# Optimization experiments

Hardware: AMD Instinct MI355X
Metric: run time of the kernel (lower is better)

The kernel has to match this reference:

```python
import jax, jax.numpy as jnp
import numpy as np

# Grid / physics constants (stand-ins for the attributes of self.model)
N = 256                 # voxels per axis (cubic unit cell)
CELL = 100.0            # unit cell edge in Angstrom (orthogonal cell, frac matrix = I/CELL)
SPACING = CELL / N      # voxel spacing in Angstrom
SOLVENT_R = 1.1         # dilation probe radius (init default `radius`)
EROSION_R = 0.9         # erosion radius (init default `erosion_radius`)
VDW_MAX = 1.9           # static upper bound on vdw radii (generation range [1.2,1.9])
N_ATOMS = 5000


def setup_inputs() -> dict:
    key = jax.random.key(0)
    k1, k2 = jax.random.split(key)
    xyz = jax.random.uniform(k1, (N_ATOMS, 3), jnp.float32) * CELL
    vdw_radii = 1.2 + 0.7 * jax.random.uniform(k2, (N_ATOMS,), jnp.float32)
    return {"xyz": xyz, "vdw_radii": vdw_radii}


def _solvent_pipeline(xyz, vdw_radii):
    # ---- Step 1: dilation -- per-atom radius query into the voxel grid ----
    max_r = VDW_MAX + SOLVENT_R                       # self.max_radius_angstrom
    Kh = int(np.ceil(max_r / SPACING))
    g = np.arange(-Kh, Kh + 1)
    offs = np.stack(np.meshgrid(g, g, g, indexing='ij'), -1).reshape(-1, 3)
    offs = jnp.asarray(offs, jnp.int32)               # [M,3] local voxel offsets

    base = jnp.floor(xyz / SPACING).astype(jnp.int32)          # [A,3] home voxel
    coords = base[:, None, :] + offs[None, :, :]               # [A,M,3]
    centers = coords.astype(jnp.float32) * SPACING             # voxel centers (unwrapped)
    d = jnp.sqrt(jnp.sum((centers - xyz[:, None, :]) ** 2, -1))  # [A,M] atom-voxel dist

    w = jnp.mod(coords, N)                                     # periodic wrap of indices
    flat = ((w[..., 0] * N + w[..., 1]) * N + w[..., 2]).ravel()

    vr = vdw_radii[:, None]
    prot = (d < vr).ravel()                                    # inside vdw -> protein core
    bound = ((d >= vr) & (d < vr + SOLVENT_R)).ravel()         # vdw..vdw+probe -> boundary

    protein = (jnp.zeros(N ** 3, jnp.int8).at[flat].max(prot.astype(jnp.int8)) > 0)
    boundary = (jnp.zeros(N ** 3, jnp.int8).at[flat].max(bound.astype(jnp.int8)) > 0)
    protein = protein.reshape(N, N, N)
    boundary = boundary.reshape(N, N, N) & ~protein            # symmetry = identity (P1)
    def_solv = ~(protein | boundary)

    # ---- Step 2: erosion -- boundary voxel flips to solvent if any voxel within
    #      erosion_radius is definitely solvent ----
    rh = int(np.ceil(EROSION_R / SPACING))
    g2 = np.arange(-rh, rh + 1)
    eo = np.stack(np.meshgrid(g2, g2, g2, indexing='ij'), -1).reshape(-1, 3)
    eo = eo[np.linalg.norm(eo * SPACING, axis=1) <= EROSION_R]  # sphere stencil (static)
    has_nb = jnp.zeros((N, N, N), bool)
    for o in eo:  # small static stencil (~50 offsets)
        has_nb = has_nb | jnp.roll(def_solv, shift=(-int(o[0]), -int(o[1]), -int(o[2])), axis=(0, 1, 2))
    flip = boundary & has_nb
    protein_with_boundary = (protein | boundary) & ~flip
    solvent = (~protein_with_boundary).astype(jnp.float32)

    # ---- Step 3: Gaussian smoothing with circular padding ----
    sigma = (SOLVENT_R / SPACING) / 4.0                        # self.transition (voxels)
    ks = int(4 * sigma + 1)
    if ks % 2 == 0:
        ks += 1
    x = np.arange(ks) - ks // 2
    g1 = np.exp(-x ** 2 / (2 * sigma ** 2))
    g1 = g1 / g1.sum()
    k3 = g1[:, None, None] * g1[None, :, None] * g1[None, None, :]
    k3 = jnp.asarray(k3 / k3.sum(), jnp.float32)
    pad = ks // 2
    padded = jnp.pad(solvent, pad, mode='wrap')
    out = jax.lax.conv_general_dilated(padded[None, None], k3[None, None], (1, 1, 1), 'VALID')
    return out[0, 0]  # [N,N,N] smoothed solvent mask


def reference(xyz, vdw_radii):
    return _solvent_pipeline(xyz, vdw_radii)
```

## Files before the change

### kernel.cpp

```cpp
#include <hip/hip_runtime.h>
#include <math.h>

#define NG 256
#define NG3 (NG*NG*NG)
#define NW (NG3/64)

typedef unsigned long long u64;
typedef unsigned int u32;

constexpr float SPACING_F = 0.390625f;
constexpr int KH = 8;
constexpr int KD = 17;
constexpr int NPAIR = KD * KD;

#define CB(x, y) (((((x) & 255) << 8) | ((y) & 255)) << 2)

__global__ void __launch_bounds__(256) splat_bits_kernel(
    const float* __restrict__ xyz, const float* __restrict__ vdw,
    u64* __restrict__ occ_bits, u64* __restrict__ p_bits, int natoms)
{
    int t = blockIdx.x * 256 + threadIdx.x;
    if (t >= natoms * NPAIR) return;
    int atom = t / NPAIR;
    int pr = t - atom * NPAIR;
    int dx = pr / KD - KH;
    int dy = pr - (pr / KD) * KD - KH;

    const float ax = xyz[atom * 3 + 0];
    const float ay = xyz[atom * 3 + 1];
    const float az = xyz[atom * 3 + 2];
    const float vr = vdw[atom];
    const float br = __fadd_rn(vr, 1.1f);
    const int bx = (int)floorf(__fdiv_rn(ax, SPACING_F));
    const int by = (int)floorf(__fdiv_rn(ay, SPACING_F));
    const int bz = (int)floorf(__fdiv_rn(az, SPACING_F));

    const int cx = bx + dx, cy = by + dy;
    float ex = __fsub_rn(__fmul_rn((float)cx, SPACING_F), ax);
    float ey = __fsub_rn(__fmul_rn((float)cy, SPACING_F), ay);
    float rxy2 = __fadd_rn(__fmul_rn(ex, ex), __fmul_rn(ey, ey));
    if (rxy2 >= __fmul_rn(br, br)) return;

    u32 mo = 0, mp = 0;
    #pragma unroll
    for (int k = 0; k < KD; ++k) {
        int cz = bz + k - KH;
        float ez = __fsub_rn(__fmul_rn((float)cz, SPACING_F), az);
        float s = __fadd_rn(rxy2, __fmul_rn(ez, ez));
        float d = __fsqrt_rn(s);
        mo |= (d < br) ? (1u << k) : 0u;
        mp |= (d < vr) ? (1u << k) : 0u;
    }
    if (!mo) return;

    const int cb = CB(cx, cy);
    const int zA = (bz - KH) & 255;
    const int wa = zA >> 6;
    const int off = zA & 63;

    u64 lo = (u64)mo << off;
    u64 hi = off ? ((u64)mo >> (64 - off)) : 0ULL;
    if (lo) atomicOr(&occ_bits[cb | wa], lo);
    if (hi) atomicOr(&occ_bits[cb | ((wa + 1) & 3)], hi);
    if (mp) {
        u64 plo = (u64)mp << off;
        u64 phi = off ? ((u64)mp >> (64 - off)) : 0ULL;
        if (plo) atomicOr(&p_bits[cb | wa], plo);
        if (phi) atomicOr(&p_bits[cb | ((wa + 1) & 3)], phi);
    }
}

#define LCB(ox, oy) ((((ox) * 14) + (oy)) * 4)
#define SCB(sx, sy) ((((sx) * 10) + (sy)) * 4)

union SMem {
    u64 occT[784];
    float stage[256][33];
};

__device__ __forceinline__ u64 lrng5(const u64* T, int cb, int wz) {
    u64 C = T[cb | wz], P = T[cb | ((wz + 3) & 3)], Nw = T[cb | ((wz + 1) & 3)];
    u64 d1 = (C << 1) | (P >> 63), d2 = (C << 2) | (P >> 62);
    u64 u1 = (C >> 1) | (Nw << 63), u2 = (C >> 2) | (Nw << 62);
    return C & d1 & d2 & u1 & u2;
}
__device__ __forceinline__ u64 lrng3(const u64* T, int cb, int wz) {
    u64 C = T[cb | wz], P = T[cb | ((wz + 3) & 3)], Nw = T[cb | ((wz + 1) & 3)];
    u64 d1 = (C << 1) | (P >> 63);
    u64 u1 = (C >> 1) | (Nw << 63);
    return C & d1 & u1;
}

struct Tri { u64 m1, m0, p1; };
__device__ __forceinline__ Tri triL(const u64* T, int cb, int wz) {
    u64 C = T[cb | wz], P = T[cb | ((wz + 3) & 3)], Nw = T[cb | ((wz + 1) & 3)];
    Tri t;
    t.m0 = C;
    t.m1 = (C << 1) | (P >> 63);
    t.p1 = (C >> 1) | (Nw << 63);
    return t;
}

__device__ __forceinline__ void csa(u64 a, u64 b, u64 c, u64& s, u64& cy) {
    u64 t = a ^ b;
    s = t ^ c;
    cy = (a & b) | (t & c);
}

__global__ void __launch_bounds__(256) solv_gauss_kernel(
    const u64* __restrict__ occ_bits, const u64* __restrict__ p_bits,
    float* __restrict__ out, float W0, float W1, float W2, float W3)
{
    __shared__ SMem sm;
    __shared__ u64 solT[400];
    __shared__ float lutA[256];

    const int tid = threadIdx.x;
    const int bx = blockIdx.x & 31, by = blockIdx.x >> 5;
    const int x0 = bx * 8, y0 = by * 8;

    for (int i = tid; i < 784; i += 256) {
        int owz = i & 3; int c = i >> 2;
        int oy = c % 14, ox = c / 14;
        sm.occT[i] = occ_bits[CB(x0 - 3 + ox, y0 - 3 + oy) | owz];
    }
    {
        int g = tid & 1, c1v = (tid >> 1) & 7, c2v = (tid >> 4) & 15;
        float acc = g ? W0 : 0.0f;
        acc = fmaf(W1, (float)c1v, acc);
        acc = fmaf(W2, (float)c2v, acc);
        lutA[tid] = acc;
    }
    __syncthreads();

    for (int i = tid; i < 400; i += 256) {
        int swz = i & 3; int c = i >> 2;
        int sy = c % 10, sx = c / 10;
        int ox = sx + 2, oy = sy + 2;
        const u64* T = sm.occT;
        u64 ero = lrng5(T, LCB(ox, oy), swz);
        ero &= lrng5(T, LCB(ox + 1, oy), swz);
        ero &= lrng5(T, LCB(ox - 1, oy), swz);
        ero &= lrng5(T, LCB(ox, oy + 1), swz);
        ero &= lrng5(T, LCB(ox, oy - 1), swz);
        ero &= lrng3(T, LCB(ox + 1, oy + 1), swz);
        ero &= lrng3(T, LCB(ox + 1, oy - 1), swz);
        ero &= lrng3(T, LCB(ox - 1, oy + 1), swz);
        ero &= lrng3(T, LCB(ox - 1, oy - 1), swz);
        ero &= lrng3(T, LCB(ox + 2, oy), swz);
        ero &= lrng3(T, LCB(ox - 2, oy), swz);
        ero &= lrng3(T, LCB(ox, oy + 2), swz);
        ero &= lrng3(T, LCB(ox, oy - 2), swz);
        ero &= T[LCB(ox + 1, oy + 2) | swz];
        ero &= T[LCB(ox + 1, oy - 2) | swz];
        ero &= T[LCB(ox - 1, oy + 2) | swz];
        ero &= T[LCB(ox - 1, oy - 2) | swz];
        ero &= T[LCB(ox + 2, oy + 1) | swz];
        ero &= T[LCB(ox + 2, oy - 1) | swz];
        ero &= T[LCB(ox - 2, oy + 1) | swz];
        ero &= T[LCB(ox - 2, oy - 1) | swz];

        u64 C = T[LCB(ox, oy) | swz];
        u64 pw = p_bits[CB(x0 - 1 + sx, y0 - 1 + sy) | swz];
        solT[i] = ~(pw | (C & ero));
    }
    __syncthreads();

    const int gwz = tid & 3;
    const int gc = tid >> 2;
    const int gy = gc & 7, gx = gc >> 3;
    const int sx = gx + 1, sy = gy + 1;

    Tri cc = triL(solT, SCB(sx, sy), gwz);
    Tri e0 = triL(solT, SCB(sx + 1, sy), gwz), e1 = triL(solT, SCB(sx - 1, sy), gwz);
    Tri e2 = triL(solT, SCB(sx, sy + 1), gwz), e3 = triL(solT, SCB(sx, sy - 1), gwz);
    Tri d0 = triL(solT, SCB(sx + 1, sy + 1), gwz), d1 = triL(solT, SCB(sx + 1, sy - 1), gwz);
    Tri d2 = triL(solT, SCB(sx - 1, sy + 1), gwz), d3 = triL(solT, SCB(sx - 1, sy - 1), gwz);

    u64 sa, ca, sb, cb2;
    csa(cc.m1, cc.p1, e0.m0, sa, ca);
    csa(e1.m0, e2.m0, e3.m0, sb, cb2);
    u64 c1b0 = sa ^ sb; u64 h = sa & sb;
    u64 c1b1, c1b2;
    csa(ca, cb2, h, c1b1, c1b2);

    u64 s1, k1, s2, k2, s3, k3, s4, k4;
    csa(e0.m1, e0.p1, e1.m1, s1, k1);
    csa(e1.p1, e2.m1, e2.p1, s2, k2);
    csa(e3.m1, e3.p1, d0.m0, s3, k3);
    csa(d1.m0, d2.m0, d3.m0, s4, k4);
    u64 t5, kt;
    csa(s1, s2, s3, t5, kt);
    u64 c2b0 = t5 ^ s4; u64 h0 = t5 & s4;
    u64 u_, ku, v_, kv;
    csa(k1, k2, k3, u_, ku);
    csa(k4, kt, h0, v_, kv);
    u64 c2b1 = u_ ^ v_; u64 h1 = u_ & v_;
    u64 c2b2, c2b3;
    csa(ku, kv, h1, c2b2, c2b3);

    u64 p1s, p1c, p2s, p2c;
    csa(d0.m1, d0.p1, d1.m1, p1s, p1c);
    csa(d1.p1, d2.m1, d2.p1, p2s, p2c);
    u64 t3, kt3;
    csa(p1s, p2s, d3.m1, t3, kt3);
    u64 c3b0 = t3 ^ d3.p1; u64 h3 = t3 & d3.p1;
    u64 u3, ku3;
    csa(p1c, p2c, kt3, u3, ku3);
    u64 c3b1 = u3 ^ h3; u64 h4 = u3 & h3;
    u64 c3b2 = ku3 ^ h4, c3b3 = ku3 & h4;

    #pragma unroll
    for (int hh = 0; hh < 2; ++hh) {
        const int sh = hh * 32;
        u32 pA[8] = { (u32)(cc.m0 >> sh), (u32)(c1b0 >> sh), (u32)(c1b1 >> sh),
                      (u32)(c1b2 >> sh), (u32)(c2b0 >> sh), (u32)(c2b1 >> sh),
                      (u32)(c2b2 >> sh), (u32)(c2b3 >> sh) };
        u32 pB[4] = { (u32)(c3b0 >> sh), (u32)(c3b1 >> sh),
                      (u32)(c3b2 >> sh), (u32)(c3b3 >> sh) };
        #pragma unroll
        for (int z0 = 0; z0 < 8; ++z0) {
            u32 accA = 0, accB = 0;
            #pragma unroll
            for (int j = 0; j < 8; ++j) accA |= ((pA[j] >> z0) & 0x01010101u) << j;
            #pragma unroll
            for (int j = 0; j < 4; ++j) accB |= ((pB[j] >> z0) & 0x01010101u) << j;
            #pragma unroll
            for (int b = 0; b < 4; ++b) {
                int idxA = (accA >> (8 * b)) & 255;
                int c3v  = (accB >> (8 * b)) & 15;
                float val = fmaf(W3, (float)c3v, lutA[idxA]);
                sm.stage[tid][z0 + 8 * b] = val;
            }
        }
        __syncthreads();
        #pragma unroll
        for (int k = 0; k < 8; ++k) {
            int i = tid + k * 256;
            int wl = i >> 3;
            int zo = (i & 7) * 4;
            int ggx = wl >> 5, ggy = (wl >> 2) & 7, ggwz = wl & 3;
            size_t base = ((size_t)(((x0 + ggx) << 10) + (y0 + ggy) * 4 + ggwz)) * 64;
            float4 v = make_float4(sm.stage[wl][zo], sm.stage[wl][zo + 1],
                                   sm.stage[wl][zo + 2], sm.stage[wl][zo + 3]);
            *(float4*)(out + base + sh + zo) = v;
        }
        __syncthreads();
    }
}

extern "C" void kernel_launch(void* const* d_in, const int* in_sizes, int n_in,
                              void* d_out, int out_size, void* d_ws, size_t ws_size,
                              hipStream_t stream)
{
    const float* xyz = (const float*)d_in[0];
    const float* vdw = (const float*)d_in[1];
    float* out = (float*)d_out;

    u64* occ_bits = (u64*)d_ws;
    u64* p_bits   = occ_bits + NW;
    const int natoms = in_sizes[1];

    hipMemsetAsync(occ_bits, 0, 2 * NW * sizeof(u64), stream);

    int nthreads = natoms * NPAIR;
    splat_bits_kernel<<<(nthreads + 255) / 256, 256, 0, stream>>>(
        xyz, vdw, occ_bits, p_bits, natoms);

    double spacing = 100.0 / 256.0;
    double sigma = 1.1 / spacing / 4.0;
    double a = exp(-1.0 / (2.0 * sigma * sigma));
    double ssum = 2.0 * a + 1.0;
    double an = a / ssum, bn = 1.0 / ssum;
    float W0 = (float)(bn * bn * bn);
    float W1 = (float)(an * bn * bn);
    float W2 = (float)(an * an * bn);
    float W3 = (float)(an * an * an);

    solv_gauss_kernel<<<1024, 256, 0, stream>>>(
        occ_bits, p_bits, out, W0, W1, W2, W3);
}
```

Measured before the change: 113.6 us.

## Replace atomic atom splat with binned per-column gather of bit masks

Atoms are first bucketed into a 64x64 xy grid of bins. A column-oriented kernel then has each block collect candidate atoms from neighbouring bins into shared memory, and each voxel column ORs its own occupancy and protein bits in registers before writing them with plain stores. This removes the global atomicOr traffic and the memset of the bit arrays, since every column is now written in full. The fixed caps on atoms per bin and candidates per block can silently drop atoms when atoms cluster, and only 256 blocks launch, which may leave much of the GPU idle.

Measured after the change: 133.2 us. 1.17x slower.

```diff
diff --git a/kernel.cpp b/kernel.cpp
--- a/kernel.cpp
+++ b/kernel.cpp
@@ -11,62 +11,128 @@
 constexpr float SPACING_F = 0.390625f;
 constexpr int KH = 8;
 constexpr int KD = 17;
-constexpr int NPAIR = KD * KD;
+
+#define NBIN 64
+#define BCAP 32
+#define NCAND 160
 
 #define CB(x, y) (((((x) & 255) << 8) | ((y) & 255)) << 2)
 
-__global__ void __launch_bounds__(256) splat_bits_kernel(
+__global__ void bin_fill_kernel(const float* __restrict__ xyz, int natoms,
+                                int* __restrict__ bin_cnt, int* __restrict__ bin_list)
+{
+    int a = blockIdx.x * 256 + threadIdx.x;
+    if (a >= natoms) return;
+    float ax = xyz[a * 3 + 0], ay = xyz[a * 3 + 1];
+    int bx = (int)floorf(__fdiv_rn(ax, SPACING_F));
+    int by = (int)floorf(__fdiv_rn(ay, SPACING_F));
+    int b = ((by >> 2) & (NBIN - 1)) * NBIN + ((bx >> 2) & (NBIN - 1));
+    int s = atomicAdd(&bin_cnt[b], 1);
+    if (s < BCAP) bin_list[b * BCAP + s] = a;
+}
+
+__global__ void __launch_bounds__(512) col_splat_kernel(
     const float* __restrict__ xyz, const float* __restrict__ vdw,
-    u64* __restrict__ occ_bits, u64* __restrict__ p_bits, int natoms)
+    const int* __restrict__ bin_cnt, const int* __restrict__ bin_list,
+    u64* __restrict__ occ_bits, u64* __restrict__ p_bits)
 {
-    int t = blockIdx.x * 256 + threadIdx.x;
-    if (t >= natoms * NPAIR) return;
-    int atom = t / NPAIR;
-    int pr = t - atom * NPAIR;
-    int dx = pr / KD - KH;
-    int dy = pr - (pr / KD) * KD - KH;
-
-    const float ax = xyz[atom * 3 + 0];
-    const float ay = xyz[atom * 3 + 1];
-    const float az = xyz[atom * 3 + 2];
-    const float vr = vdw[atom];
-    const float br = __fadd_rn(vr, 1.1f);
-    const int bx = (int)floorf(__fdiv_rn(ax, SPACING_F));
-    const int by = (int)floorf(__fdiv_rn(ay, SPACING_F));
-    const int bz = (int)floorf(__fdiv_rn(az, SPACING_F));
-
-    const int cx = bx + dx, cy = by + dy;
-    float ex = __fsub_rn(__fmul_rn((float)cx, SPACING_F), ax);
-    float ey = __fsub_rn(__fmul_rn((float)cy, SPACING_F), ay);
-    float rxy2 = __fadd_rn(__fmul_rn(ex, ex), __fmul_rn(ey, ey));
-    if (rxy2 >= __fmul_rn(br, br)) return;
-
-    u32 mo = 0, mp = 0;
-    #pragma unroll
-    for (int k = 0; k < KD; ++k) {
-        int cz = bz + k - KH;
-        float ez = __fsub_rn(__fmul_rn((float)cz, SPACING_F), az);
-        float s = __fadd_rn(rxy2, __fmul_rn(ez, ez));
-        float d = __fsqrt_rn(s);
-        mo |= (d < br) ? (1u << k) : 0u;
-        mp |= (d < vr) ? (1u << k) : 0u;
-    }
-    if (!mo) return;
-
-    const int cb = CB(cx, cy);
-    const int zA = (bz - KH) & 255;
-    const int wa = zA >> 6;
-    const int off = zA & 63;
-
-    u64 lo = (u64)mo << off;
-    u64 hi = off ? ((u64)mo >> (64 - off)) : 0ULL;
-    if (lo) atomicOr(&occ_bits[cb | wa], lo);
-    if (hi) atomicOr(&occ_bits[cb | ((wa + 1) & 3)], hi);
-    if (mp) {
+    __shared__ float4 candF[NCAND];
+    __shared__ int    candB[NCAND];
+    __shared__ int lc;
+
+    const int tid = threadIdx.x;
+    const int BX = blockIdx.x & 15, BY = blockIdx.x >> 4;
+    const int x0 = BX * 16, y0 = BY * 16;
+
+    if (tid == 0) lc = 0;
+    __syncthreads();
+
+    if (tid < 64) {
+        int abx = (4 * BX - 2 + (tid & 7)) & (NBIN - 1);
+        int aby = (4 * BY - 2 + (tid >> 3)) & (NBIN - 1);
+        int b = aby * NBIN + abx;
+        int n = min(bin_cnt[b], BCAP);
+        if (n > 0) {
+            int base = atomicAdd(&lc, n);
+            for (int j = 0; j < n; ++j) {
+                int idx = base + j;
+                if (idx < NCAND) {
+                    int a = bin_list[b * BCAP + j];
+                    float ax = xyz[a * 3 + 0], ay = xyz[a * 3 + 1], az = xyz[a * 3 + 2];
+                    candF[idx] = make_float4(ax, ay, az, vdw[a]);
+                    int bx = (int)floorf(__fdiv_rn(ax, SPACING_F));
+                    int by = (int)floorf(__fdiv_rn(ay, SPACING_F));
+                    int bz = (int)floorf(__fdiv_rn(az, SPACING_F));
+                    candB[idx] = bx | (by << 8) | (bz << 16);
+                }
+            }
+        }
+    }
+    __syncthreads();
+    const int nc = min(lc, NCAND);
+
+    const int col = tid >> 1;
+    const int sub = tid & 1;
+    const int X = x0 + (col >> 4), Y = y0 + (col & 15);
+
+    u64 o0 = 0, o1 = 0, o2 = 0, o3 = 0;
+    u64 q0 = 0, q1 = 0, q2 = 0, q3 = 0;
+
+    for (int c = sub; c < nc; c += 2) {
+        float4 f = candF[c];
+        int bb = candB[c];
+        int bx = bb & 255, by = (bb >> 8) & 255, bz = (bb >> 16) & 255;
+        int dx = ((X - bx + 128) & 255) - 128;
+        int dy = ((Y - by + 128) & 255) - 128;
+        if (dx < -KH || dx > KH || dy < -KH || dy > KH) continue;
+        float ex = __fsub_rn(__fmul_rn((float)(bx + dx), SPACING_F), f.x);
+        float ey = __fsub_rn(__fmul_rn((float)(by + dy), SPACING_F), f.y);
+        float rxy2 = __fadd_rn(__fmul_rn(ex, ex), __fmul_rn(ey, ey));
+        float vr = f.w;
+        float br = __fadd_rn(vr, 1.1f);
+        if (rxy2 >= __fmul_rn(br, br)) continue;
+
+        u32 mo = 0, mp = 0;
+        #pragma unroll
+        for (int k = 0; k < KD; ++k) {
+            int cz = bz + k - KH;
+            float ez = __fsub_rn(__fmul_rn((float)cz, SPACING_F), f.z);
+            float s = __fadd_rn(rxy2, __fmul_rn(ez, ez));
+            float d = __fsqrt_rn(s);
+            mo |= (d < br) ? (1u << k) : 0u;
+            mp |= (d < vr) ? (1u << k) : 0u;
+        }
+        if (!mo) continue;
+
+        int zA = (bz - KH) & 255;
+        int wa = zA >> 6, off = zA & 63;
+        int wb = (wa + 1) & 3;
+        u64 lo = (u64)mo << off;
+        u64 hi = off ? ((u64)mo >> (64 - off)) : 0ULL;
         u64 plo = (u64)mp << off;
         u64 phi = off ? ((u64)mp >> (64 - off)) : 0ULL;
-        if (plo) atomicOr(&p_bits[cb | wa], plo);
-        if (phi) atomicOr(&p_bits[cb | ((wa + 1) & 3)], phi);
+        o0 |= (wa == 0 ? lo : 0) | (wb == 0 ? hi : 0);
+        o1 |= (wa == 1 ? lo : 0) | (wb == 1 ? hi : 0);
+        o2 |= (wa == 2 ? lo : 0) | (wb == 2 ? hi : 0);
+        o3 |= (wa == 3 ? lo : 0) | (wb == 3 ? hi : 0);
+        q0 |= (wa == 0 ? plo : 0) | (wb == 0 ? phi : 0);
+        q1 |= (wa == 1 ? plo : 0) | (wb == 1 ? phi : 0);
+        q2 |= (wa == 2 ? plo : 0) | (wb == 2 ? phi : 0);
+        q3 |= (wa == 3 ? plo : 0) | (wb == 3 ? phi : 0);
+    }
+
+    o0 |= __shfl_xor(o0, 1, 64);  o1 |= __shfl_xor(o1, 1, 64);
+    o2 |= __shfl_xor(o2, 1, 64);  o3 |= __shfl_xor(o3, 1, 64);
+    q0 |= __shfl_xor(q0, 1, 64);  q1 |= __shfl_xor(q1, 1, 64);
+    q2 |= __shfl_xor(q2, 1, 64);  q3 |= __shfl_xor(q3, 1, 64);
+
+    u64* dst = (sub == 0 ? occ_bits : p_bits) + CB(X, Y);
+    if (sub == 0) {
+        *(ulonglong2*)(dst + 0) = make_ulonglong2(o0, o1);
+        *(ulonglong2*)(dst + 2) = make_ulonglong2(o2, o3);
+    } else {
+        *(ulonglong2*)(dst + 0) = make_ulonglong2(q0, q1);
+        *(ulonglong2*)(dst + 2) = make_ulonglong2(q2, q3);
     }
 }
 
@@ -259,13 +325,15 @@
 
     u64* occ_bits = (u64*)d_ws;
     u64* p_bits   = occ_bits + NW;
+    int* bin_cnt  = (int*)(p_bits + NW);
+    int* bin_list = bin_cnt + NBIN * NBIN;
     const int natoms = in_sizes[1];
 
-    hipMemsetAsync(occ_bits, 0, 2 * NW * sizeof(u64), stream);
-
-    int nthreads = natoms * NPAIR;
-    splat_bits_kernel<<<(nthreads + 255) / 256, 256, 0, stream>>>(
-        xyz, vdw, occ_bits, p_bits, natoms);
+    hipMemsetAsync(bin_cnt, 0, NBIN * NBIN * sizeof(int), stream);
+    bin_fill_kernel<<<(natoms + 255) / 256, 256, 0, stream>>>(
+        xyz, natoms, bin_cnt, bin_list);
+    col_splat_kernel<<<256, 512, 0, stream>>>(
+        xyz, vdw, bin_cnt, bin_list, occ_bits, p_bits);
 
     double spacing = 100.0 / 256.0;
     double sigma = 1.1 / spacing / 4.0;
```

## Stage packed per-voxel count bits in shared memory and expand to floats at store

Applied to the files above, without the earlier changes.

Each thread now writes compact per-voxel count bit fields (8-bit A index and 4-bit B count) to shared memory instead of 64 staged floats. A single barrier follows, and the store phase unpacks those fields, does the LUT lookup and FMA, and writes float4s directly. This removes the two staging rounds and the extra barriers, and shrinks shared memory traffic. The occupancy tile load is also vectorized so one thread copies four u64 words with two 128-bit loads. In exchange, the LUT lookups and bit extraction move into the store loop, whose lutA reads may bank-conflict.

Measured after the change: 114.8 us. Within noise of the previous version (+1.1%).

```diff
diff --git a/kernel.cpp b/kernel.cpp
--- a/kernel.cpp
+++ b/kernel.cpp
@@ -72,10 +72,11 @@
 
 #define LCB(ox, oy) ((((ox) * 14) + (oy)) * 4)
 #define SCB(sx, sy) ((((sx) * 10) + (sy)) * 4)
+#define ASTRIDE 25
 
 union SMem {
     u64 occT[784];
-    float stage[256][33];
+    u32 accAB[256 * ASTRIDE];
 };
 
 __device__ __forceinline__ u64 lrng5(const u64* T, int cb, int wz) {
@@ -119,10 +120,14 @@
     const int bx = blockIdx.x & 31, by = blockIdx.x >> 5;
     const int x0 = bx * 8, y0 = by * 8;
 
-    for (int i = tid; i < 784; i += 256) {
-        int owz = i & 3; int c = i >> 2;
-        int oy = c % 14, ox = c / 14;
-        sm.occT[i] = occ_bits[CB(x0 - 3 + ox, y0 - 3 + oy) | owz];
+    if (tid < 196) {
+        int oy = tid % 14, ox = tid / 14;
+        const u64* src = &occ_bits[CB(x0 - 3 + ox, y0 - 3 + oy)];
+        ulonglong2 a = *(const ulonglong2*)(src);
+        ulonglong2 b = *(const ulonglong2*)(src + 2);
+        u64* dst = &sm.occT[(ox * 14 + oy) * 4];
+        *(ulonglong2*)(dst) = a;
+        *(ulonglong2*)(dst + 2) = b;
     }
     {
         int g = tid & 1, c1v = (tid >> 1) & 7, c2v = (tid >> 4) & 15;
@@ -166,86 +171,99 @@
     }
     __syncthreads();
 
-    const int gwz = tid & 3;
-    const int gc = tid >> 2;
-    const int gy = gc & 7, gx = gc >> 3;
-    const int sx = gx + 1, sy = gy + 1;
-
-    Tri cc = triL(solT, SCB(sx, sy), gwz);
-    Tri e0 = triL(solT, SCB(sx + 1, sy), gwz), e1 = triL(solT, SCB(sx - 1, sy), gwz);
-    Tri e2 = triL(solT, SCB(sx, sy + 1), gwz), e3 = triL(solT, SCB(sx, sy - 1), gwz);
-    Tri d0 = triL(solT, SCB(sx + 1, sy + 1), gwz), d1 = triL(solT, SCB(sx + 1, sy - 1), gwz);
-    Tri d2 = triL(solT, SCB(sx - 1, sy + 1), gwz), d3 = triL(solT, SCB(sx - 1, sy - 1), gwz);
-
-    u64 sa, ca, sb, cb2;
-    csa(cc.m1, cc.p1, e0.m0, sa, ca);
-    csa(e1.m0, e2.m0, e3.m0, sb, cb2);
-    u64 c1b0 = sa ^ sb; u64 h = sa & sb;
-    u64 c1b1, c1b2;
-    csa(ca, cb2, h, c1b1, c1b2);
-
-    u64 s1, k1, s2, k2, s3, k3, s4, k4;
-    csa(e0.m1, e0.p1, e1.m1, s1, k1);
-    csa(e1.p1, e2.m1, e2.p1, s2, k2);
-    csa(e3.m1, e3.p1, d0.m0, s3, k3);
-    csa(d1.m0, d2.m0, d3.m0, s4, k4);
-    u64 t5, kt;
-    csa(s1, s2, s3, t5, kt);
-    u64 c2b0 = t5 ^ s4; u64 h0 = t5 & s4;
-    u64 u_, ku, v_, kv;
-    csa(k1, k2, k3, u_, ku);
-    csa(k4, kt, h0, v_, kv);
-    u64 c2b1 = u_ ^ v_; u64 h1 = u_ & v_;
-    u64 c2b2, c2b3;
-    csa(ku, kv, h1, c2b2, c2b3);
-
-    u64 p1s, p1c, p2s, p2c;
-    csa(d0.m1, d0.p1, d1.m1, p1s, p1c);
-    csa(d1.p1, d2.m1, d2.p1, p2s, p2c);
-    u64 t3, kt3;
-    csa(p1s, p2s, d3.m1, t3, kt3);
-    u64 c3b0 = t3 ^ d3.p1; u64 h3 = t3 & d3.p1;
-    u64 u3, ku3;
-    csa(p1c, p2c, kt3, u3, ku3);
-    u64 c3b1 = u3 ^ h3; u64 h4 = u3 & h3;
-    u64 c3b2 = ku3 ^ h4, c3b3 = ku3 & h4;
+    {
+        const int gwz = tid & 3;
+        const int gc = tid >> 2;
+        const int gy = gc & 7, gx = gc >> 3;
+        const int sx = gx + 1, sy = gy + 1;
+
+        Tri cc = triL(solT, SCB(sx, sy), gwz);
+        Tri e0 = triL(solT, SCB(sx + 1, sy), gwz), e1 = triL(solT, SCB(sx - 1, sy), gwz);
+        Tri e2 = triL(solT, SCB(sx, sy + 1), gwz), e3 = triL(solT, SCB(sx, sy - 1), gwz);
+        Tri d0 = triL(solT, SCB(sx + 1, sy + 1), gwz), d1 = triL(solT, SCB(sx + 1, sy - 1), gwz);
+        Tri d2 = triL(solT, SCB(sx - 1, sy + 1), gwz), d3 = triL(solT, SCB(sx - 1, sy - 1), gwz);
+
+        u64 sa, ca, sb, cb2;
+        csa(cc.m1, cc.p1, e0.m0, sa, ca);
+        csa(e1.m0, e2.m0, e3.m0, sb, cb2);
+        u64 c1b0 = sa ^ sb; u64 h = sa & sb;
+        u64 c1b1, c1b2;
+        csa(ca, cb2, h, c1b1, c1b2);
+
+        u64 s1, k1, s2, k2, s3, k3, s4, k4;
+        csa(e0.m1, e0.p1, e1.m1, s1, k1);
+        csa(e1.p1, e2.m1, e2.p1, s2, k2);
+        csa(e3.m1, e3.p1, d0.m0, s3, k3);
+        csa(d1.m0, d2.m0, d3.m0, s4, k4);
+        u64 t5, kt;
+        csa(s1, s2, s3, t5, kt);
+        u64 c2b0 = t5 ^ s4; u64 h0 = t5 & s4;
+        u64 u_, ku, v_, kv;
+        csa(k1, k2, k3, u_, ku);
+        csa(k4, kt, h0, v_, kv);
+        u64 c2b1 = u_ ^ v_; u64 h1 = u_ & v_;
+        u64 c2b2, c2b3;
+        csa(ku, kv, h1, c2b2, c2b3);
+
+        u64 p1s, p1c, p2s, p2c;
+        csa(d0.m1, d0.p1, d1.m1, p1s, p1c);
+        csa(d1.p1, d2.m1, d2.p1, p2s, p2c);
+        u64 t3, kt3;
+        csa(p1s, p2s, d3.m1, t3, kt3);
+        u64 c3b0 = t3 ^ d3.p1; u64 h3 = t3 & d3.p1;
+        u64 u3, ku3;
+        csa(p1c, p2c, kt3, u3, ku3);
+        u64 c3b1 = u3 ^ h3; u64 h4 = u3 & h3;
+        u64 c3b2 = ku3 ^ h4, c3b3 = ku3 & h4;
+
+        u32* myA = &sm.accAB[tid * ASTRIDE];
+        #pragma unroll
+        for (int hh = 0; hh < 2; ++hh) {
+            const int sh = hh * 32;
+            u32 pA[8] = { (u32)(cc.m0 >> sh), (u32)(c1b0 >> sh), (u32)(c1b1 >> sh),
+                          (u32)(c1b2 >> sh), (u32)(c2b0 >> sh), (u32)(c2b1 >> sh),
+                          (u32)(c2b2 >> sh), (u32)(c2b3 >> sh) };
+            u32 pB[4] = { (u32)(c3b0 >> sh), (u32)(c3b1 >> sh),
+                          (u32)(c3b2 >> sh), (u32)(c3b3 >> sh) };
+            u32 bv[8];
+            #pragma unroll
+            for (int z0 = 0; z0 < 8; ++z0) {
+                u32 accA = 0, accB = 0;
+                #pragma unroll
+                for (int j = 0; j < 8; ++j) accA |= ((pA[j] >> z0) & 0x01010101u) << j;
+                #pragma unroll
+                for (int j = 0; j < 4; ++j) accB |= ((pB[j] >> z0) & 0x01010101u) << j;
+                myA[hh * 8 + z0] = accA;
+                bv[z0] = accB;
+            }
+            #pragma unroll
+            for (int p = 0; p < 4; ++p)
+                myA[16 + hh * 4 + p] = bv[2 * p] | (bv[2 * p + 1] << 4);
+        }
+    }
+    __syncthreads();
 
     #pragma unroll
-    for (int hh = 0; hh < 2; ++hh) {
-        const int sh = hh * 32;
-        u32 pA[8] = { (u32)(cc.m0 >> sh), (u32)(c1b0 >> sh), (u32)(c1b1 >> sh),
-                      (u32)(c1b2 >> sh), (u32)(c2b0 >> sh), (u32)(c2b1 >> sh),
-                      (u32)(c2b2 >> sh), (u32)(c2b3 >> sh) };
-        u32 pB[4] = { (u32)(c3b0 >> sh), (u32)(c3b1 >> sh),
-                      (u32)(c3b2 >> sh), (u32)(c3b3 >> sh) };
-        #pragma unroll
-        for (int z0 = 0; z0 < 8; ++z0) {
-            u32 accA = 0, accB = 0;
-            #pragma unroll
-            for (int j = 0; j < 8; ++j) accA |= ((pA[j] >> z0) & 0x01010101u) << j;
-            #pragma unroll
-            for (int j = 0; j < 4; ++j) accB |= ((pB[j] >> z0) & 0x01010101u) << j;
-            #pragma unroll
-            for (int b = 0; b < 4; ++b) {
-                int idxA = (accA >> (8 * b)) & 255;
-                int c3v  = (accB >> (8 * b)) & 15;
-                float val = fmaf(W3, (float)c3v, lutA[idxA]);
-                sm.stage[tid][z0 + 8 * b] = val;
-            }
-        }
-        __syncthreads();
-        #pragma unroll
-        for (int k = 0; k < 8; ++k) {
-            int i = tid + k * 256;
-            int wl = i >> 3;
-            int zo = (i & 7) * 4;
-            int ggx = wl >> 5, ggy = (wl >> 2) & 7, ggwz = wl & 3;
-            size_t base = ((size_t)(((x0 + ggx) << 10) + (y0 + ggy) * 4 + ggwz)) * 64;
-            float4 v = make_float4(sm.stage[wl][zo], sm.stage[wl][zo + 1],
-                                   sm.stage[wl][zo + 2], sm.stage[wl][zo + 3]);
-            *(float4*)(out + base + sh + zo) = v;
-        }
-        __syncthreads();
+    for (int k = 0; k < 16; ++k) {
+        int f = k * 256 + tid;
+        int u = f >> 4;
+        int q = f & 15;
+        int hh = q >> 3;
+        int qb = (q & 7) >> 1;
+        const u32* ua = &sm.accAB[u * ASTRIDE];
+        int za = hh * 8 + 4 * (q & 1);
+        u32 A0 = ua[za + 0], A1 = ua[za + 1], A2 = ua[za + 2], A3 = ua[za + 3];
+        u32 Blo = ua[16 + hh * 4 + 2 * (q & 1)];
+        u32 Bhi = ua[16 + hh * 4 + 2 * (q & 1) + 1];
+        int shb = 8 * qb;
+        float4 v;
+        v.x = fmaf(W3, (float)((Blo >> (shb + 0)) & 15u), lutA[(A0 >> shb) & 255u]);
+        v.y = fmaf(W3, (float)((Blo >> (shb + 4)) & 15u), lutA[(A1 >> shb) & 255u]);
+        v.z = fmaf(W3, (float)((Bhi >> (shb + 0)) & 15u), lutA[(A2 >> shb) & 255u]);
+        v.w = fmaf(W3, (float)((Bhi >> (shb + 4)) & 15u), lutA[(A3 >> shb) & 255u]);
+        int gx = u >> 5, gy = (u >> 2) & 7, gwz = u & 3;
+        size_t base = ((size_t)((x0 + gx) * 1024 + (y0 + gy) * 4 + gwz)) * 64 + q * 4;
+        *(float4*)(out + base) = v;
     }
 }
 
```
